# Kernel optimization log

Measured on AMD Instinct MI355X. Metric: run time of the kernel, lower is better.

Reference implementation:

```python
import jax, jax.numpy as jnp
import numpy as np

SIGMA_DATA = 16.0
ALPHA_BOND = 1.0


def safe_norm(x, axis=-1):
    # L2 norm with zero (sub)gradient at 0, matching torch.norm's behavior
    sq = jnp.sum(x * x, axis=axis)
    n = jnp.sqrt(jnp.where(sq > 0, sq, 1.0))
    return jnp.where(sq > 0, n, 0.0)


def weighted_rigid_align(x_l, xGT_l, w_l):
    # Aligns x_l onto xGT_l's frame (Kabsch with weights); output is detached.
    wm = w_l[..., None]                                   # [B,N,1]
    denom = jnp.sum(wm, axis=1, keepdims=True)
    mu = jnp.sum(wm * x_l, axis=1, keepdims=True) / denom
    muGT = jnp.sum(wm * xGT_l, axis=1, keepdims=True) / denom
    xc = x_l - mu
    xGTc = xGT_l - muGT
    # M = (w * xGT_c)^T @ x_c  -> [B,3,3]
    M = jnp.einsum('bni,bnj->bij', wm * xGTc, xc)
    U, S, Vh = jnp.linalg.svd(M)
    R = U @ Vh
    det = jnp.linalg.det(R)
    Fm = jnp.array([[1.0, 0.0, 0.0], [0.0, 1.0, 0.0], [0.0, 0.0, -1.0]], dtype=R.dtype)
    Rfix = jnp.einsum('bij,jk,bkl->bil', U, Fm, Vh)
    R = jnp.where(det[:, None, None] < 0, Rfix, R)
    xalign = xc @ jnp.swapaxes(R, -1, -2) + muGT
    return jax.lax.stop_gradient(xalign)


def diffusion_loss(xpred_l, xGT_l, ht, w_l):
    # Align ground truth onto prediction (note arg order in original forward)
    xGT_aligned = weighted_rigid_align(xGT_l, xpred_l, w_l)
    loss = jnp.sum(safe_norm(xpred_l - xGT_aligned) * w_l) / jnp.sum(w_l)
    if ALPHA_BOND > 0:
        w_pair = w_l[:, :, None] * w_l[:, None, :]                 # [B,N,N]
        d_pred = safe_norm(xpred_l[:, :, None] - xpred_l[:, None]) # [B,N,N]
        d_gt = safe_norm(xGT_l[:, :, None] - xGT_l[:, None])       # [B,N,N]
        L_bond = w_pair * (d_pred - d_gt) ** 2
        loss = loss + ALPHA_BOND * jnp.sum(L_bond) / jnp.sum(w_pair)
    return (ht ** 2 + SIGMA_DATA ** 2) / (ht + SIGMA_DATA) ** 2 * loss


def setup_inputs() -> dict:
    key = jax.random.key(0)
    k1, k2, k3, k4 = jax.random.split(key, 4)
    B, N = 4, 2048
    xpred_l = jax.random.normal(k1, (B, N, 3), dtype=jnp.float32) * 10.0
    xGT_l = jax.random.normal(k2, (B, N, 3), dtype=jnp.float32) * 10.0
    ht = jax.random.uniform(k3, (B,), dtype=jnp.float32, minval=0.1, maxval=4.0)
    w_l = jax.random.uniform(k4, (B, N), dtype=jnp.float32, minval=0.1, maxval=1.0)
    return {"xpred_l": xpred_l, "xGT_l": xGT_l, "ht": ht, "w_l": w_l}


def reference(xpred_l, xGT_l, ht, w_l):
    return diffusion_loss(xpred_l, xGT_l, ht, w_l)
```

## Files before the change

### kernel.cpp

```cpp
#include <hip/hip_runtime.h>
#include <math.h>


#define RT   256
#define TSZ  128
#define GBLK 512
#define MAXB 8
#define MAGIC 0x00C0FFEEDEADBEEFULL

__device__ __forceinline__ void flag_set(unsigned long long* p) {
    __hip_atomic_store(p, (unsigned long long)MAGIC, __ATOMIC_RELEASE,
                       __HIP_MEMORY_SCOPE_AGENT);
}
__device__ __forceinline__ void flag_wait(unsigned long long* p) {
    while (__hip_atomic_load(p, __ATOMIC_ACQUIRE, __HIP_MEMORY_SCOPE_AGENT)
           != (unsigned long long)MAGIC)
        __builtin_amdgcn_s_sleep(1);
}
__device__ __forceinline__ void dstore(double* p, double v) {
    __hip_atomic_store((unsigned long long*)p, __double_as_longlong(v),
                       __ATOMIC_RELAXED, __HIP_MEMORY_SCOPE_AGENT);
}
__device__ __forceinline__ double dload(const double* p) {
    return __longlong_as_double(
        __hip_atomic_load((const unsigned long long*)p, __ATOMIC_RELAXED,
                          __HIP_MEMORY_SCOPE_AGENT));
}

__global__ __launch_bounds__(RT, 2)
void k_fused(const float* __restrict__ pred, const float* __restrict__ gt,
             const float* __restrict__ ht, const float* __restrict__ w,
             float* __restrict__ out, double* __restrict__ ws,
             int N, int B, int CT, int T, int TT, int SPB, int SB) {
    const int tid  = threadIdx.x;
    const int blk  = blockIdx.x;
    const int lane = tid & 63, wave = tid >> 6;

    double*             statsData = ws;
    unsigned long long* statsFlag = (unsigned long long*)(statsData + (size_t)SB*16);
    double*             Rdata     = (double*)(statsFlag + SB);
    unsigned long long* Rflag     = (unsigned long long*)(Rdata + (size_t)B*16);
    double*             partData  = (double*)(Rflag + B);
    unsigned long long* partFlag  = (unsigned long long*)(partData + (size_t)GBLK*2);

    __shared__ float4 sp4[TSZ], sg4[TSZ];
    __shared__ double shred[4][16];
    __shared__ double sstat[16];
    __shared__ float  sR[MAXB][15];
    __shared__ double sW[MAXB];

    if (blk < SB) {
        const int b = blk / SPB, j = blk - b*SPB;
        const int n = j*RT + tid;
        float px=0.f,py=0.f,pz=0.f,gx=0.f,gy=0.f,gz=0.f,wn=0.f;
        if (n < N) {
            const float* p = pred + (size_t)b*N*3;
            const float* g = gt   + (size_t)b*N*3;
            px = p[3*n]; py = p[3*n+1]; pz = p[3*n+2];
            gx = g[3*n]; gy = g[3*n+1]; gz = g[3*n+2];
            wn = w[(size_t)b*N + n];
        }
        double wd=wn, pxd=px,pyd=py,pzd=pz, gxd=gx,gyd=gy,gzd=gz;
        double st[16] = {wd, wd*pxd, wd*pyd, wd*pzd, wd*gxd, wd*gyd, wd*gzd,
                         wd*pxd*gxd, wd*pxd*gyd, wd*pxd*gzd,
                         wd*pyd*gxd, wd*pyd*gyd, wd*pyd*gzd,
                         wd*pzd*gxd, wd*pzd*gyd, wd*pzd*gzd};
        #pragma unroll
        for (int off = 32; off > 0; off >>= 1) {
            #pragma unroll
            for (int k = 0; k < 16; k++) st[k] += __shfl_down(st[k], off, 64);
        }
        if (lane == 0) {
            #pragma unroll
            for (int k = 0; k < 16; k++) shred[wave][k] = st[k];
        }
        __syncthreads();
        if (tid < 16)
            dstore(&statsData[(size_t)blk*16 + tid],
                   shred[0][tid]+shred[1][tid]+shred[2][tid]+shred[3][tid]);
        __syncthreads();
        if (tid == 0) { __threadfence(); flag_set(&statsFlag[blk]); }
    }

    double bd = 0.0;
    {
        const int NB = GBLK - B;
        int tlist[3]; int ntl = 0;
        if (blk < NB && blk < TT) tlist[ntl++] = blk;
        if (blk >= SB && blk < NB) {
            const int stride = NB - SB;
            for (int t = NB + (blk - SB); t < TT && ntl < 3; t += stride)
                tlist[ntl++] = t;
        }
        for (int ti = 0; ti < ntl; ti++) {
            const int t = tlist[ti];
            const int b = t / T;
            int rem = t - b*T, bx = 0;
            while (rem >= CT - bx) { rem -= (CT - bx); bx++; }
            const int by = bx + rem;
            const int r0 = bx*TSZ, c0 = by*TSZ;
            const float* p  = pred + (size_t)b*N*3;
            const float* g  = gt   + (size_t)b*N*3;
            const float* wb = w    + (size_t)b*N;

            __syncthreads();
            {
                const int i = tid & (TSZ - 1);
                const int m = c0 + i;
                if (tid < TSZ) {
                    float4 v = make_float4(0.f,0.f,0.f,0.f);
                    if (m < N) v = make_float4(p[3*m], p[3*m+1], p[3*m+2], wb[m]);
                    sp4[i] = v;
                } else {
                    float4 v = make_float4(0.f,0.f,0.f,0.f);
                    if (m < N) v = make_float4(g[3*m], g[3*m+1], g[3*m+2], 0.f);
                    sg4[i] = v;
                }
            }
            __syncthreads();

            const int rrow  = tid & (TSZ - 1);
            const int rhalf = tid >> 7;
            const int n     = r0 + rrow;
            float px=0.f,py=0.f,pz=0.f,gx=0.f,gy=0.f,gz=0.f,wn=0.f;
            if (n < N) {
                px = p[3*n]; py = p[3*n+1]; pz = p[3*n+2];
                gx = g[3*n]; gy = g[3*n+1]; gz = g[3*n+2];
                wn = wb[n];
            }
            float acc = 0.f;
            const int ib = rhalf * (TSZ/2);
            if (by > bx) {
                #pragma unroll 4
                for (int jj = 0; jj < TSZ/2; jj++) {
                    const int i = ib + jj;
                    float4 cp = sp4[i], cg = sg4[i];
                    float dxp=px-cp.x, dyp=py-cp.y, dzp=pz-cp.z;
                    float dxg=gx-cg.x, dyg=gy-cg.y, dzg=gz-cg.z;
                    float dp = sqrtf(dxp*dxp+dyp*dyp+dzp*dzp);
                    float dg = sqrtf(dxg*dxg+dyg*dyg+dzg*dzg);
                    float dd = dp - dg;
                    acc = fmaf(cp.w, dd*dd, acc);
                }
            } else {
                #pragma unroll 4
                for (int jj = 0; jj < TSZ/2; jj++) {
                    const int i = ib + jj;
                    float4 cp = sp4[i], cg = sg4[i];
                    float dxp=px-cp.x, dyp=py-cp.y, dzp=pz-cp.z;
                    float dxg=gx-cg.x, dyg=gy-cg.y, dzg=gz-cg.z;
                    float dp = sqrtf(dxp*dxp+dyp*dyp+dzp*dzp);
                    float dg = sqrtf(dxg*dxg+dyg*dyg+dzg*dzg);
                    float dd = dp - dg;
                    float tt = cp.w * (dd*dd);
                    acc += (i > rrow) ? tt : 0.f;
                }
            }
            bd += (double)(2.0f * wn * acc);
        }
    }

    if (blk >= GBLK - B) {
        const int b = blk - (GBLK - B);
        if (tid < SPB) flag_wait(&statsFlag[b*SPB + tid]);
        __syncthreads();
        if (tid < 16) {
            double acc = 0.0;
            for (int j = 0; j < SPB; j++)
                acc += dload(&statsData[((size_t)b*SPB + j)*16 + tid]);
            sstat[tid] = acc;
        }
        __syncthreads();
        if (tid == 0) {
            const double* s = sstat;
            double W = s[0];
            double mup[3] = { s[1]/W, s[2]/W, s[3]/W };
            double mug[3] = { s[4]/W, s[5]/W, s[6]/W };
            double M[3][3];
            for (int i = 0; i < 3; i++)
                for (int j = 0; j < 3; j++)
                    M[i][j] = s[7 + i*3 + j] - W * mup[i] * mug[j];
            double A[3][3];
            for (int i = 0; i < 3; i++)
                for (int j = 0; j < 3; j++) {
                    double tacc = 0.0;
                    for (int k = 0; k < 3; k++) tacc += M[k][i] * M[k][j];
                    A[i][j] = tacc;
                }
            double V[3][3] = {{1,0,0},{0,1,0},{0,0,1}};
            for (int sweep = 0; sweep < 6; sweep++) {
                for (int pq = 0; pq < 3; pq++) {
                    int pp_ = (pq == 2) ? 1 : 0;
                    int qq_ = (pq == 0) ? 1 : 2;
                    double apq = A[pp_][qq_];
                    if (fabs(apq) < 1e-300) continue;
                    double app = A[pp_][pp_], aqq = A[qq_][qq_];
                    double theta = (aqq - app) / (2.0 * apq);
                    double tj = copysign(1.0, theta) / (fabs(theta) + sqrt(theta*theta + 1.0));
                    double cj = 1.0 / sqrt(tj*tj + 1.0), sn = tj * cj;
                    A[pp_][pp_] = app - tj * apq;
                    A[qq_][qq_] = aqq + tj * apq;
                    A[pp_][qq_] = A[qq_][pp_] = 0.0;
                    int r = 3 - pp_ - qq_;
                    double arp = A[r][pp_], arq = A[r][qq_];
                    A[r][pp_] = A[pp_][r] = cj*arp - sn*arq;
                    A[r][qq_] = A[qq_][r] = sn*arp + cj*arq;
                    for (int rr = 0; rr < 3; rr++) {
                        double vp = V[rr][pp_], vq = V[rr][qq_];
                        V[rr][pp_] = cj*vp - sn*vq;
                        V[rr][qq_] = sn*vp + cj*vq;
                    }
                }
            }
            double d[3] = { A[0][0], A[1][1], A[2][2] };
            int idx[3] = {0, 1, 2};
            for (int i = 0; i < 2; i++)
                for (int j = i + 1; j < 3; j++)
                    if (d[idx[j]] > d[idx[i]]) { int tt2 = idx[i]; idx[i] = idx[j]; idx[j] = tt2; }
            double u[3][3], v[3][3];
            for (int i = 0; i < 3; i++) {
                int c_ = idx[i];
                double sv = sqrt(fmax(d[c_], 0.0));
                double inv = (sv > 1e-12) ? 1.0 / sv : 0.0;
                for (int r = 0; r < 3; r++) v[i][r] = V[r][c_];
                for (int r = 0; r < 3; r++) {
                    double tacc = 0.0;
                    for (int k = 0; k < 3; k++) tacc += M[r][k] * v[i][k];
                    u[i][r] = tacc * inv;
                }
            }
            double detM = M[0][0]*(M[1][1]*M[2][2] - M[1][2]*M[2][1])
                        - M[0][1]*(M[1][0]*M[2][2] - M[1][2]*M[2][0])
                        + M[0][2]*(M[1][0]*M[2][1] - M[1][1]*M[2][0]);
            double sg2 = (detM < 0.0) ? -1.0 : 1.0;
            for (int r = 0; r < 3; r++)
                for (int c2 = 0; c2 < 3; c2++)
                    dstore(&Rdata[(size_t)b*16 + r*3 + c2],
                           u[0][r]*v[0][c2] + u[1][r]*v[1][c2] + sg2 * u[2][r]*v[2][c2]);
            for (int i = 0; i < 3; i++) dstore(&Rdata[(size_t)b*16 + 9 + i],  mup[i]);
            for (int i = 0; i < 3; i++) dstore(&Rdata[(size_t)b*16 + 12 + i], mug[i]);
            dstore(&Rdata[(size_t)b*16 + 15], W);
            __threadfence();
            flag_set(&Rflag[b]);
        }
    }

    if (tid < B) flag_wait(&Rflag[tid]);
    __syncthreads();
    if (tid < B*16) {
        const int b = tid >> 4, k = tid & 15;
        double v = dload(&Rdata[(size_t)b*16 + k]);
        if (k < 15) sR[b][k] = (float)v; else sW[b] = v;
    }
    __syncthreads();

    double al = 0.0;
    const int PPB = (B*N + GBLK - 1) / GBLK;
    if (tid < PPB) {
        const int pt = blk*PPB + tid;
        if (pt < B*N) {
            const int b = pt / N, nn = pt - b*N;
            const float* pp = pred + (size_t)b*N*3;
            const float* gg = gt   + (size_t)b*N*3;
            const float* Rb = sR[b];
            float x0 = gg[3*nn]-Rb[12], x1 = gg[3*nn+1]-Rb[13], x2 = gg[3*nn+2]-Rb[14];
            float ax = fmaf(Rb[0],x0, fmaf(Rb[1],x1, fmaf(Rb[2],x2, Rb[9])));
            float ay = fmaf(Rb[3],x0, fmaf(Rb[4],x1, fmaf(Rb[5],x2, Rb[10])));
            float az = fmaf(Rb[6],x0, fmaf(Rb[7],x1, fmaf(Rb[8],x2, Rb[11])));
            float ex = pp[3*nn]-ax, ey = pp[3*nn+1]-ay, ez = pp[3*nn+2]-az;
            al = (double)(w[(size_t)b*N + nn] * sqrtf(ex*ex + ey*ey + ez*ez));
        }
    }

    #pragma unroll
    for (int off = 32; off > 0; off >>= 1) {
        al += __shfl_down(al, off, 64);
        bd += __shfl_down(bd, off, 64);
    }
    if (lane == 0) { shred[wave][0] = al; shred[wave][1] = bd; }
    __syncthreads();
    if (tid == 0) {
        dstore(&partData[(size_t)blk*2 + 0],
               shred[0][0]+shred[1][0]+shred[2][0]+shred[3][0]);
        dstore(&partData[(size_t)blk*2 + 1],
               shred[0][1]+shred[1][1]+shred[2][1]+shred[3][1]);
        __threadfence();
        flag_set(&partFlag[blk]);
    }

    if (blk == GBLK - 1) {
        double aA = 0.0, bA = 0.0;
        for (int i = tid; i < GBLK; i += RT) {
            flag_wait(&partFlag[i]);
            aA += dload(&partData[(size_t)i*2 + 0]);
            bA += dload(&partData[(size_t)i*2 + 1]);
        }
        #pragma unroll
        for (int off = 32; off > 0; off >>= 1) {
            aA += __shfl_down(aA, off, 64);
            bA += __shfl_down(bA, off, 64);
        }
        __syncthreads();
        if (lane == 0) { shred[wave][2] = aA; shred[wave][3] = bA; }
        __syncthreads();
        if (tid == 0) {
            double at = shred[0][2]+shred[1][2]+shred[2][2]+shred[3][2];
            double bt = shred[0][3]+shred[1][3]+shred[2][3]+shred[3][3];
            double tw = 0.0, twp = 0.0;
            for (int b2 = 0; b2 < B; b2++) { double W = sW[b2]; tw += W; twp += W*W; }
            double loss = at / tw + bt / twp;
            for (int b2 = 0; b2 < B; b2++) {
                double h = (double)ht[b2];
                out[b2] = (float)(((h*h + 256.0) / ((h + 16.0)*(h + 16.0))) * loss);
            }
        }
    }
}

extern "C" void kernel_launch(void* const* d_in, const int* in_sizes, int n_in,
                              void* d_out, int out_size, void* d_ws, size_t ws_size,
                              hipStream_t stream) {
    const float* pred = (const float*)d_in[0];
    const float* gt   = (const float*)d_in[1];
    const float* ht   = (const float*)d_in[2];
    const float* w    = (const float*)d_in[3];
    int B = in_sizes[2];
    int N = in_sizes[3] / B;
    double* ws = (double*)d_ws;
    float* out = (float*)d_out;

    int CTt = (N + TSZ - 1) / TSZ;
    int T   = CTt * (CTt + 1) / 2;
    int TT  = T * B;
    int SPB = (N + RT - 1) / RT;
    int SB  = B * SPB;

    k_fused<<<dim3(GBLK), dim3(RT), 0, stream>>>(pred, gt, ht, w, out, ws,
                                                 N, B, CTt, T, TT, SPB, SB);
}
```

Before: 103.8 us.

## Replace inter-block flag spinning with redundant per-block stats and atomic finish

Each alignment block now recomputes its batch's full weighted statistics and Kabsch rotation locally, so blocks no longer spin on stats and rotation flags. The remaining bond tiles go to other blocks, which take two tiles each. The final reduction uses atomicAdd with a ticket counter instead of a last block polling per-block flags, and every block recomputes the weight sums itself. This removes the cross-block waits and serial chains, but adds redundant reads of the whole batch per block, an extra memset launch, and a nondeterministic atomic summation order.

```diff
diff --git a/kernel.cpp b/kernel.cpp
--- a/kernel.cpp
+++ b/kernel.cpp
@@ -6,65 +6,117 @@
 #define TSZ  128
 #define GBLK 512
 #define MAXB 8
-#define MAGIC 0x00C0FFEEDEADBEEFULL
-
-__device__ __forceinline__ void flag_set(unsigned long long* p) {
-    __hip_atomic_store(p, (unsigned long long)MAGIC, __ATOMIC_RELEASE,
-                       __HIP_MEMORY_SCOPE_AGENT);
-}
-__device__ __forceinline__ void flag_wait(unsigned long long* p) {
-    while (__hip_atomic_load(p, __ATOMIC_ACQUIRE, __HIP_MEMORY_SCOPE_AGENT)
-           != (unsigned long long)MAGIC)
-        __builtin_amdgcn_s_sleep(1);
-}
-__device__ __forceinline__ void dstore(double* p, double v) {
-    __hip_atomic_store((unsigned long long*)p, __double_as_longlong(v),
-                       __ATOMIC_RELAXED, __HIP_MEMORY_SCOPE_AGENT);
-}
-__device__ __forceinline__ double dload(const double* p) {
-    return __longlong_as_double(
-        __hip_atomic_load((const unsigned long long*)p, __ATOMIC_RELAXED,
-                          __HIP_MEMORY_SCOPE_AGENT));
-}
 
 __global__ __launch_bounds__(RT, 2)
 void k_fused(const float* __restrict__ pred, const float* __restrict__ gt,
              const float* __restrict__ ht, const float* __restrict__ w,
              float* __restrict__ out, double* __restrict__ ws,
-             int N, int B, int CT, int T, int TT, int SPB, int SB) {
+             int N, int B, int T, int TT, int nA, int APB, int PPB, int SPT) {
     const int tid  = threadIdx.x;
     const int blk  = blockIdx.x;
     const int lane = tid & 63, wave = tid >> 6;
-
-    double*             statsData = ws;
-    unsigned long long* statsFlag = (unsigned long long*)(statsData + (size_t)SB*16);
-    double*             Rdata     = (double*)(statsFlag + SB);
-    unsigned long long* Rflag     = (unsigned long long*)(Rdata + (size_t)B*16);
-    double*             partData  = (double*)(Rflag + B);
-    unsigned long long* partFlag  = (unsigned long long*)(partData + (size_t)GBLK*2);
+    double* fin = ws;
 
     __shared__ float4 sp4[TSZ], sg4[TSZ];
     __shared__ double shred[4][16];
     __shared__ double sstat[16];
-    __shared__ float  sR[MAXB][15];
-    __shared__ double sW[MAXB];
-
-    if (blk < SB) {
-        const int b = blk / SPB, j = blk - b*SPB;
-        const int n = j*RT + tid;
-        float px=0.f,py=0.f,pz=0.f,gx=0.f,gy=0.f,gz=0.f,wn=0.f;
-        if (n < N) {
-            const float* p = pred + (size_t)b*N*3;
-            const float* g = gt   + (size_t)b*N*3;
-            px = p[3*n]; py = p[3*n+1]; pz = p[3*n+2];
-            gx = g[3*n]; gy = g[3*n+1]; gz = g[3*n+2];
-            wn = w[(size_t)b*N + n];
-        }
-        double wd=wn, pxd=px,pyd=py,pzd=pz, gxd=gx,gyd=gy,gzd=gz;
-        double st[16] = {wd, wd*pxd, wd*pyd, wd*pzd, wd*gxd, wd*gyd, wd*gzd,
-                         wd*pxd*gxd, wd*pxd*gyd, wd*pxd*gzd,
-                         wd*pyd*gxd, wd*pyd*gyd, wd*pyd*gzd,
-                         wd*pzd*gxd, wd*pzd*gyd, wd*pzd*gzd};
+    __shared__ float  sRl[15];
+
+    const bool typeA = (blk < nA);
+    const int  sb    = typeA ? (blk / APB) : 0;
+
+    const int t1 = typeA ? blk : (2*blk - nA);
+    const int t2 = typeA ? TT  : (2*blk - nA + 1);
+
+    const int CTt = (N + TSZ - 1) / TSZ;
+
+    auto decode = [&](int t, int& bb, int& r0, bool& diag, int& c0) {
+        bb = t / T;
+        int rem = t - bb*T, bx = 0;
+        while (rem >= CTt - bx) { rem -= (CTt - bx); bx++; }
+        int by = bx + rem;
+        r0 = bx*TSZ; c0 = by*TSZ; diag = (bx == by);
+    };
+    auto stage = [&](int bb, int c0) {
+        const float* p  = pred + (size_t)bb*N*3;
+        const float* g  = gt   + (size_t)bb*N*3;
+        const float* wb = w    + (size_t)bb*N;
+        const int i = tid & (TSZ - 1);
+        const int m = c0 + i;
+        if (tid < TSZ) {
+            float4 v = make_float4(0.f,0.f,0.f,0.f);
+            if (m < N) v = make_float4(p[3*m], p[3*m+1], p[3*m+2], wb[m]);
+            sp4[i] = v;
+        } else {
+            float4 v = make_float4(0.f,0.f,0.f,0.f);
+            if (m < N) v = make_float4(g[3*m], g[3*m+1], g[3*m+2], 0.f);
+            sg4[i] = v;
+        }
+    };
+    auto bond_unit = [&](int u, int bb, int r0, bool diag) -> double {
+        const int row = u & (TSZ - 1), half = u >> 7;
+        const int n = r0 + row;
+        if (n >= N) return 0.0;
+        const float* p = pred + (size_t)bb*N*3;
+        const float* g = gt   + (size_t)bb*N*3;
+        const float wn = w[(size_t)bb*N + n];
+        const float px=p[3*n], py=p[3*n+1], pz=p[3*n+2];
+        const float gx=g[3*n], gy=g[3*n+1], gz=g[3*n+2];
+        float acc = 0.f;
+        const int ib = half * (TSZ/2);
+        if (!diag) {
+            #pragma unroll 4
+            for (int jj = 0; jj < TSZ/2; jj++) {
+                const int i = ib + jj;
+                float4 cp = sp4[i], cg = sg4[i];
+                float dxp=px-cp.x, dyp=py-cp.y, dzp=pz-cp.z;
+                float dxg=gx-cg.x, dyg=gy-cg.y, dzg=gz-cg.z;
+                float dp = sqrtf(dxp*dxp+dyp*dyp+dzp*dzp);
+                float dg = sqrtf(dxg*dxg+dyg*dyg+dzg*dzg);
+                float dd = dp - dg;
+                acc = fmaf(cp.w, dd*dd, acc);
+            }
+        } else {
+            #pragma unroll 4
+            for (int jj = 0; jj < TSZ/2; jj++) {
+                const int i = ib + jj;
+                float4 cp = sp4[i], cg = sg4[i];
+                float dxp=px-cp.x, dyp=py-cp.y, dzp=pz-cp.z;
+                float dxg=gx-cg.x, dyg=gy-cg.y, dzg=gz-cg.z;
+                float dp = sqrtf(dxp*dxp+dyp*dyp+dzp*dzp);
+                float dg = sqrtf(dxg*dxg+dyg*dyg+dzg*dzg);
+                float dd = dp - dg;
+                float tt = cp.w * (dd*dd);
+                acc += (i > row) ? tt : 0.f;
+            }
+        }
+        return (double)(2.0f * wn * acc);
+    };
+
+    int b1 = 0, r01 = 0, c01 = 0; bool d1 = false;
+    if (t1 < TT) { decode(t1, b1, r01, d1, c01); stage(b1, c01); }
+
+    if (typeA) {
+        const float* p  = pred + (size_t)sb*N*3;
+        const float* g  = gt   + (size_t)sb*N*3;
+        const float* wb = w    + (size_t)sb*N;
+        double st[16];
+        #pragma unroll
+        for (int k = 0; k < 16; k++) st[k] = 0.0;
+        for (int k = 0; k < SPT; k++) {
+            const int n = tid + k*RT;
+            if (n < N) {
+                double wd = wb[n];
+                double pxd=p[3*n], pyd=p[3*n+1], pzd=p[3*n+2];
+                double gxd=g[3*n], gyd=g[3*n+1], gzd=g[3*n+2];
+                st[0] += wd;
+                st[1] += wd*pxd;  st[2] += wd*pyd;  st[3] += wd*pzd;
+                st[4] += wd*gxd;  st[5] += wd*gyd;  st[6] += wd*gzd;
+                st[7] += wd*pxd*gxd; st[8]  += wd*pxd*gyd; st[9]  += wd*pxd*gzd;
+                st[10]+= wd*pyd*gxd; st[11] += wd*pyd*gyd; st[12] += wd*pyd*gzd;
+                st[13]+= wd*pzd*gxd; st[14] += wd*pzd*gyd; st[15] += wd*pzd*gzd;
+            }
+        }
         #pragma unroll
         for (int off = 32; off > 0; off >>= 1) {
             #pragma unroll
@@ -74,103 +126,14 @@
             #pragma unroll
             for (int k = 0; k < 16; k++) shred[wave][k] = st[k];
         }
-        __syncthreads();
-        if (tid < 16)
-            dstore(&statsData[(size_t)blk*16 + tid],
-                   shred[0][tid]+shred[1][tid]+shred[2][tid]+shred[3][tid]);
-        __syncthreads();
-        if (tid == 0) { __threadfence(); flag_set(&statsFlag[blk]); }
-    }
+    }
+    __syncthreads();
+    if (typeA && tid < 16)
+        sstat[tid] = shred[0][tid]+shred[1][tid]+shred[2][tid]+shred[3][tid];
+    __syncthreads();
 
     double bd = 0.0;
-    {
-        const int NB = GBLK - B;
-        int tlist[3]; int ntl = 0;
-        if (blk < NB && blk < TT) tlist[ntl++] = blk;
-        if (blk >= SB && blk < NB) {
-            const int stride = NB - SB;
-            for (int t = NB + (blk - SB); t < TT && ntl < 3; t += stride)
-                tlist[ntl++] = t;
-        }
-        for (int ti = 0; ti < ntl; ti++) {
-            const int t = tlist[ti];
-            const int b = t / T;
-            int rem = t - b*T, bx = 0;
-            while (rem >= CT - bx) { rem -= (CT - bx); bx++; }
-            const int by = bx + rem;
-            const int r0 = bx*TSZ, c0 = by*TSZ;
-            const float* p  = pred + (size_t)b*N*3;
-            const float* g  = gt   + (size_t)b*N*3;
-            const float* wb = w    + (size_t)b*N;
-
-            __syncthreads();
-            {
-                const int i = tid & (TSZ - 1);
-                const int m = c0 + i;
-                if (tid < TSZ) {
-                    float4 v = make_float4(0.f,0.f,0.f,0.f);
-                    if (m < N) v = make_float4(p[3*m], p[3*m+1], p[3*m+2], wb[m]);
-                    sp4[i] = v;
-                } else {
-                    float4 v = make_float4(0.f,0.f,0.f,0.f);
-                    if (m < N) v = make_float4(g[3*m], g[3*m+1], g[3*m+2], 0.f);
-                    sg4[i] = v;
-                }
-            }
-            __syncthreads();
-
-            const int rrow  = tid & (TSZ - 1);
-            const int rhalf = tid >> 7;
-            const int n     = r0 + rrow;
-            float px=0.f,py=0.f,pz=0.f,gx=0.f,gy=0.f,gz=0.f,wn=0.f;
-            if (n < N) {
-                px = p[3*n]; py = p[3*n+1]; pz = p[3*n+2];
-                gx = g[3*n]; gy = g[3*n+1]; gz = g[3*n+2];
-                wn = wb[n];
-            }
-            float acc = 0.f;
-            const int ib = rhalf * (TSZ/2);
-            if (by > bx) {
-                #pragma unroll 4
-                for (int jj = 0; jj < TSZ/2; jj++) {
-                    const int i = ib + jj;
-                    float4 cp = sp4[i], cg = sg4[i];
-                    float dxp=px-cp.x, dyp=py-cp.y, dzp=pz-cp.z;
-                    float dxg=gx-cg.x, dyg=gy-cg.y, dzg=gz-cg.z;
-                    float dp = sqrtf(dxp*dxp+dyp*dyp+dzp*dzp);
-                    float dg = sqrtf(dxg*dxg+dyg*dyg+dzg*dzg);
-                    float dd = dp - dg;
-                    acc = fmaf(cp.w, dd*dd, acc);
-                }
-            } else {
-                #pragma unroll 4
-                for (int jj = 0; jj < TSZ/2; jj++) {
-                    const int i = ib + jj;
-                    float4 cp = sp4[i], cg = sg4[i];
-                    float dxp=px-cp.x, dyp=py-cp.y, dzp=pz-cp.z;
-                    float dxg=gx-cg.x, dyg=gy-cg.y, dzg=gz-cg.z;
-                    float dp = sqrtf(dxp*dxp+dyp*dyp+dzp*dzp);
-                    float dg = sqrtf(dxg*dxg+dyg*dyg+dzg*dzg);
-                    float dd = dp - dg;
-                    float tt = cp.w * (dd*dd);
-                    acc += (i > rrow) ? tt : 0.f;
-                }
-            }
-            bd += (double)(2.0f * wn * acc);
-        }
-    }
-
-    if (blk >= GBLK - B) {
-        const int b = blk - (GBLK - B);
-        if (tid < SPB) flag_wait(&statsFlag[b*SPB + tid]);
-        __syncthreads();
-        if (tid < 16) {
-            double acc = 0.0;
-            for (int j = 0; j < SPB; j++)
-                acc += dload(&statsData[((size_t)b*SPB + j)*16 + tid]);
-            sstat[tid] = acc;
-        }
-        __syncthreads();
+    if (typeA) {
         if (tid == 0) {
             const double* s = sstat;
             double W = s[0];
@@ -235,40 +198,48 @@
             double sg2 = (detM < 0.0) ? -1.0 : 1.0;
             for (int r = 0; r < 3; r++)
                 for (int c2 = 0; c2 < 3; c2++)
-                    dstore(&Rdata[(size_t)b*16 + r*3 + c2],
-                           u[0][r]*v[0][c2] + u[1][r]*v[1][c2] + sg2 * u[2][r]*v[2][c2]);
-            for (int i = 0; i < 3; i++) dstore(&Rdata[(size_t)b*16 + 9 + i],  mup[i]);
-            for (int i = 0; i < 3; i++) dstore(&Rdata[(size_t)b*16 + 12 + i], mug[i]);
-            dstore(&Rdata[(size_t)b*16 + 15], W);
-            __threadfence();
-            flag_set(&Rflag[b]);
-        }
-    }
-
-    if (tid < B) flag_wait(&Rflag[tid]);
+                    sRl[r*3 + c2] = (float)(u[0][r]*v[0][c2] + u[1][r]*v[1][c2]
+                                            + sg2 * u[2][r]*v[2][c2]);
+            for (int i = 0; i < 3; i++) sRl[9 + i]  = (float)mup[i];
+            for (int i = 0; i < 3; i++) sRl[12 + i] = (float)mug[i];
+        } else if (tid >= 64) {
+            const int q = tid - 64;
+            bd += bond_unit(q, b1, r01, d1);
+            if (q < 64) bd += bond_unit(q + 192, b1, r01, d1);
+        }
+    } else {
+        if (t1 < TT) bd += bond_unit(tid, b1, r01, d1);
+        __syncthreads();
+        int b2t = 0, r02 = 0, c02 = 0; bool d2 = false;
+        if (t2 < TT) { decode(t2, b2t, r02, d2, c02); stage(b2t, c02); }
+        __syncthreads();
+        if (t2 < TT) bd += bond_unit(tid, b2t, r02, d2);
+    }
     __syncthreads();
-    if (tid < B*16) {
-        const int b = tid >> 4, k = tid & 15;
-        double v = dload(&Rdata[(size_t)b*16 + k]);
-        if (k < 15) sR[b][k] = (float)v; else sW[b] = v;
-    }
-    __syncthreads();
 
     double al = 0.0;
-    const int PPB = (B*N + GBLK - 1) / GBLK;
-    if (tid < PPB) {
-        const int pt = blk*PPB + tid;
-        if (pt < B*N) {
-            const int b = pt / N, nn = pt - b*N;
-            const float* pp = pred + (size_t)b*N*3;
-            const float* gg = gt   + (size_t)b*N*3;
-            const float* Rb = sR[b];
-            float x0 = gg[3*nn]-Rb[12], x1 = gg[3*nn+1]-Rb[13], x2 = gg[3*nn+2]-Rb[14];
-            float ax = fmaf(Rb[0],x0, fmaf(Rb[1],x1, fmaf(Rb[2],x2, Rb[9])));
-            float ay = fmaf(Rb[3],x0, fmaf(Rb[4],x1, fmaf(Rb[5],x2, Rb[10])));
-            float az = fmaf(Rb[6],x0, fmaf(Rb[7],x1, fmaf(Rb[8],x2, Rb[11])));
-            float ex = pp[3*nn]-ax, ey = pp[3*nn+1]-ay, ez = pp[3*nn+2]-az;
-            al = (double)(w[(size_t)b*N + nn] * sqrtf(ex*ex + ey*ey + ez*ez));
+    if (typeA && tid < PPB) {
+        const int n = (blk - sb*APB)*PPB + tid;
+        if (n < N) {
+            const float* pp = pred + (size_t)sb*N*3;
+            const float* gg = gt   + (size_t)sb*N*3;
+            float x0 = gg[3*n]-sRl[12], x1 = gg[3*n+1]-sRl[13], x2 = gg[3*n+2]-sRl[14];
+            float ax = fmaf(sRl[0],x0, fmaf(sRl[1],x1, fmaf(sRl[2],x2, sRl[9])));
+            float ay = fmaf(sRl[3],x0, fmaf(sRl[4],x1, fmaf(sRl[5],x2, sRl[10])));
+            float az = fmaf(sRl[6],x0, fmaf(sRl[7],x1, fmaf(sRl[8],x2, sRl[11])));
+            float ex = pp[3*n]-ax, ey = pp[3*n+1]-ay, ez = pp[3*n+2]-az;
+            al = (double)(w[(size_t)sb*N + n] * sqrtf(ex*ex + ey*ey + ez*ez));
+        }
+    }
+
+    double wsum[MAXB];
+    #pragma unroll
+    for (int b2 = 0; b2 < MAXB; b2++) wsum[b2] = 0.0;
+    #pragma unroll
+    for (int b2 = 0; b2 < MAXB; b2++) {
+        if (b2 < B) {
+            const float* wb = w + (size_t)b2*N;
+            for (int n = tid; n < N; n += RT) wsum[b2] += (double)wb[n];
         }
     }
 
@@ -276,38 +247,35 @@
     for (int off = 32; off > 0; off >>= 1) {
         al += __shfl_down(al, off, 64);
         bd += __shfl_down(bd, off, 64);
-    }
-    if (lane == 0) { shred[wave][0] = al; shred[wave][1] = bd; }
+        #pragma unroll
+        for (int b2 = 0; b2 < MAXB; b2++)
+            wsum[b2] += __shfl_down(wsum[b2], off, 64);
+    }
+    if (lane == 0) {
+        shred[wave][0] = al;
+        shred[wave][1] = bd;
+        #pragma unroll
+        for (int b2 = 0; b2 < MAXB; b2++) shred[wave][2 + b2] = wsum[b2];
+    }
     __syncthreads();
     if (tid == 0) {
-        dstore(&partData[(size_t)blk*2 + 0],
-               shred[0][0]+shred[1][0]+shred[2][0]+shred[3][0]);
-        dstore(&partData[(size_t)blk*2 + 1],
-               shred[0][1]+shred[1][1]+shred[2][1]+shred[3][1]);
+        double alB = shred[0][0]+shred[1][0]+shred[2][0]+shred[3][0];
+        double bdB = shred[0][1]+shred[1][1]+shred[2][1]+shred[3][1];
+        double tw = 0.0, twp = 0.0;
+        #pragma unroll
+        for (int b2 = 0; b2 < MAXB; b2++) {
+            if (b2 < B) {
+                double W = shred[0][2+b2]+shred[1][2+b2]+shred[2][2+b2]+shred[3][2+b2];
+                tw += W; twp += W*W;
+            }
+        }
+        atomicAdd(&fin[0], alB);
+        atomicAdd(&fin[1], bdB);
         __threadfence();
-        flag_set(&partFlag[blk]);
-    }
-
-    if (blk == GBLK - 1) {
-        double aA = 0.0, bA = 0.0;
-        for (int i = tid; i < GBLK; i += RT) {
-            flag_wait(&partFlag[i]);
-            aA += dload(&partData[(size_t)i*2 + 0]);
-            bA += dload(&partData[(size_t)i*2 + 1]);
-        }
-        #pragma unroll
-        for (int off = 32; off > 0; off >>= 1) {
-            aA += __shfl_down(aA, off, 64);
-            bA += __shfl_down(bA, off, 64);
-        }
-        __syncthreads();
-        if (lane == 0) { shred[wave][2] = aA; shred[wave][3] = bA; }
-        __syncthreads();
-        if (tid == 0) {
-            double at = shred[0][2]+shred[1][2]+shred[2][2]+shred[3][2];
-            double bt = shred[0][3]+shred[1][3]+shred[2][3]+shred[3][3];
-            double tw = 0.0, twp = 0.0;
-            for (int b2 = 0; b2 < B; b2++) { double W = sW[b2]; tw += W; twp += W*W; }
+        unsigned old = atomicAdd((unsigned int*)&fin[2], 1u);
+        if (old == (unsigned)(GBLK - 1)) {
+            double at = atomicAdd(&fin[0], 0.0);
+            double bt = atomicAdd(&fin[1], 0.0);
             double loss = at / tw + bt / twp;
             for (int b2 = 0; b2 < B; b2++) {
                 double h = (double)ht[b2];
@@ -332,9 +300,13 @@
     int CTt = (N + TSZ - 1) / TSZ;
     int T   = CTt * (CTt + 1) / 2;
     int TT  = T * B;
-    int SPB = (N + RT - 1) / RT;
-    int SB  = B * SPB;
-
+    int nB  = (TT > GBLK) ? (TT - GBLK) : 0;
+    int nA  = GBLK - nB;
+    int APB = nA / B;
+    int PPB = (N + APB - 1) / APB;
+    int SPT = (N + RT - 1) / RT;
+
+    hipMemsetAsync(ws, 0, 3 * sizeof(double), stream);
     k_fused<<<dim3(GBLK), dim3(RT), 0, stream>>>(pred, gt, ht, w, out, ws,
-                                                 N, B, CTt, T, TT, SPB, SB);
+                                                 N, B, T, TT, nA, APB, PPB, SPT);
 }
```

Measured after the change: 111.6 us. 1.08x slower.
